# Performance work log

Hardware: AMD Instinct MI355X
Metric: run time of the kernel (lower is better)

The kernel has to match this reference:

```python
import jax, jax.numpy as jnp
import numpy as np

N = 100000
E = 1600000
F = 64
OUT = 7

def setup_inputs() -> dict:
    key = jax.random.key(0)
    k1, k2, k3, k4, k5 = jax.random.split(key, 5)
    x = jax.random.normal(k1, (N, F), dtype=jnp.float32)
    edge_index = jax.random.randint(k2, (2, E), 0, N, dtype=jnp.int64)
    W_l = jax.random.normal(k3, (F, OUT), dtype=jnp.float32) / np.sqrt(F)
    b_l = jax.random.normal(k4, (OUT,), dtype=jnp.float32) * 0.01
    W_r = jax.random.normal(k5, (F, OUT), dtype=jnp.float32) / np.sqrt(F)
    return {"x": x, "edge_index": edge_index, "W_l": W_l, "b_l": b_l, "W_r": W_r}

def reference(x, edge_index, W_l, b_l, W_r):
    # PyG SAGEConv (mean aggr): out = lin_l(mean_{j in N(i)} x_j) + lin_r(x_i), then relu
    src, dst = edge_index[0], edge_index[1]
    msgs = x[src]                                            # [E, F] gather
    agg = jax.ops.segment_sum(msgs, dst, num_segments=N)     # [N, F]
    cnt = jax.ops.segment_sum(jnp.ones((E,), dtype=x.dtype), dst, num_segments=N)
    mean = agg / jnp.maximum(cnt, 1.0)[:, None]              # isolated nodes -> 0
    out = mean @ W_l + b_l + x @ W_r                         # [N, 7]
    return jax.nn.relu(out)
```

## Files before the change

kernel.cpp:

```cpp
#include <hip/hip_runtime.h>

#define NN 100000
#define NE 1600000
#define FIN 64
#define FOUT 7

#define BSH 9
#define NBK 196
#define PBLK 2000
#define PTH  256
#define EPB  800
#define NCOPY 4
#define NCTR (NBK * NCOPY)
#define ROWS 200
#define SPLIT 4
#define NTASK (NBK * SPLIT)
#define RPS (PBLK / SPLIT)
#define ATH 512
#define WSLOT 12
#define OVCAP 256
#define SCAP 3968
#define PROJB 391
#define INVALID 0xFFFFFFFFu

__device__ __forceinline__ unsigned bf16r(float f) {
    unsigned u = __float_as_uint(f);
    return (u + 0x7fffu + ((u >> 16) & 1u)) >> 16;
}
__device__ __forceinline__ float bflo(unsigned u) { return __uint_as_float(u << 16); }
__device__ __forceinline__ float bfhi(unsigned u) { return __uint_as_float(u & 0xffff0000u); }

__global__ __launch_bounds__(256) void proj_kernel(
    const float* __restrict__ x, const float* __restrict__ Wl,
    const float* __restrict__ bl, const float* __restrict__ Wr,
    unsigned* __restrict__ z, float* __restrict__ outself, int n)
{
    int i = blockIdx.x * blockDim.x + threadIdx.x;
    if (i >= n) return;

    float al[FOUT], ar[FOUT];
#pragma unroll
    for (int j = 0; j < FOUT; ++j) { al[j] = 0.f; ar[j] = 0.f; }

    const float4* xr = (const float4*)(x + (size_t)i * FIN);
#pragma unroll
    for (int kk = 0; kk < FIN / 4; ++kk) {
        float4 xv = xr[kk];
        float v[4] = {xv.x, xv.y, xv.z, xv.w};
#pragma unroll
        for (int c = 0; c < 4; ++c) {
            int k = kk * 4 + c;
#pragma unroll
            for (int j = 0; j < FOUT; ++j) {
                al[j] = fmaf(v[c], Wl[k * FOUT + j], al[j]);
                ar[j] = fmaf(v[c], Wr[k * FOUT + j], ar[j]);
            }
        }
    }

    uint4 pk;
    pk.x = bf16r(al[0]) | (bf16r(al[1]) << 16);
    pk.y = bf16r(al[2]) | (bf16r(al[3]) << 16);
    pk.z = bf16r(al[4]) | (bf16r(al[5]) << 16);
    pk.w = bf16r(al[6]);
    ((uint4*)z)[i] = pk;

    float* o = outself + (size_t)i * FOUT;
#pragma unroll
    for (int j = 0; j < FOUT; ++j)
        o[j] = ar[j] + bl[j];
}

__global__ __launch_bounds__(PTH) void part_kernel(
    const int* __restrict__ eg, unsigned* __restrict__ part,
    unsigned short* __restrict__ offs)
{
    __shared__ unsigned st_cnt[NCTR];
    __shared__ unsigned st_start[NCTR];
    __shared__ unsigned stage[EPB];
    __shared__ unsigned wsum[NCOPY];

    const int t    = threadIdx.x;
    const int e0   = (int)blockIdx.x * EPB;
    const int lane = t & 63;
    const int wv   = t >> 6;

    for (int b = t; b < NCTR; b += PTH) st_cnt[b] = 0;
    __syncthreads();

    unsigned held[4], hcr[4];
#pragma unroll
    for (int q = 0; q < 4; ++q) hcr[q] = INVALID;
    if (t < EPB / 4) {
        uint4 S = *(const uint4*)(eg + e0 + 4 * t);
        uint4 D = *(const uint4*)(eg + NE + e0 + 4 * t);
        unsigned ss[4] = {S.x, S.y, S.z, S.w};
        unsigned dd[4] = {D.x, D.y, D.z, D.w};
#pragma unroll
        for (int q = 0; q < 4; ++q) {
            unsigned b = dd[q] >> BSH;
            unsigned cidx = (unsigned)wv * NBK + b;
            unsigned r = atomicAdd(&st_cnt[cidx], 1u);
            held[q] = ((dd[q] & 511u) << 17) | ss[q];
            hcr[q]  = (cidx << 10) | r;
        }
    }
    __syncthreads();

    unsigned c[4], p[4], tot = 0;
    if (t < NBK) {
#pragma unroll
        for (int w = 0; w < NCOPY; ++w) c[w] = st_cnt[w * NBK + t];
        p[0] = 0; p[1] = c[0]; p[2] = c[0] + c[1]; p[3] = p[2] + c[2];
        tot = p[3] + c[3];
    }
    unsigned inc = tot;
#pragma unroll
    for (int off = 1; off < 64; off <<= 1) {
        unsigned v = (unsigned)__shfl_up((int)inc, off, 64);
        if (lane >= off) inc += v;
    }
    if (lane == 63) wsum[wv] = inc;
    __syncthreads();
    if (t == 0) {
        unsigned run = 0;
#pragma unroll
        for (int w = 0; w < NCOPY; ++w) { unsigned tmp = wsum[w]; wsum[w] = run; run += tmp; }
    }
    __syncthreads();
    unsigned bstart = wsum[wv] + inc - tot;
    if (t < NBK) {
        offs[(size_t)blockIdx.x * ROWS + t] = (unsigned short)bstart;
#pragma unroll
        for (int w = 0; w < NCOPY; ++w) st_start[w * NBK + t] = bstart + p[w];
    }
    if (t == NBK) offs[(size_t)blockIdx.x * ROWS + NBK] = (unsigned short)EPB;
    __syncthreads();

#pragma unroll
    for (int q = 0; q < 4; ++q) {
        if (hcr[q] != INVALID) {
            unsigned cidx = hcr[q] >> 10, r = hcr[q] & 0x3FFu;
            stage[st_start[cidx] + r] = held[q];
        }
    }
    __syncthreads();

    const uint4* sg = (const uint4*)stage;
    uint4* pg = (uint4*)(part + (size_t)blockIdx.x * EPB);
    for (int j = t; j < EPB / 4; j += PTH) pg[j] = sg[j];
}

__global__ __launch_bounds__(ATH) void acc_kernel(
    const unsigned short* __restrict__ offs, const unsigned* __restrict__ part,
    const unsigned* __restrict__ zb, float* __restrict__ partial)
{
    __shared__ unsigned s_cnt[512];
    __shared__ unsigned s_start[512];
    __shared__ __align__(16) unsigned sstage[SCAP + 8];
    __shared__ unsigned ovf[2 * OVCAP];
    __shared__ unsigned novf;
    __shared__ unsigned wtot[8];

    const int t    = threadIdx.x;
    const int lane = t & 63;
    const int k    = blockIdx.x >> 2;
    const int sp   = blockIdx.x & 3;

    s_cnt[t] = 0;
    if (t == 0) novf = 0;
    __syncthreads();

    unsigned rbase = 0, len = 0;
    if (t < RPS) {
        unsigned r = (unsigned)(sp * RPS + t);
        unsigned o0 = offs[(size_t)r * ROWS + k];
        unsigned o1 = offs[(size_t)r * ROWS + k + 1];
        len   = o1 - o0;
        rbase = r * EPB + o0;
    }

    unsigned sh = rbase & 3u;
    const uint4* p4 = (const uint4*)part;
    unsigned wbase = rbase >> 2;
    uint4 W0 = len ? p4[wbase]     : make_uint4(0, 0, 0, 0);
    uint4 W1 = len ? p4[wbase + 1] : make_uint4(0, 0, 0, 0);
    uint4 W2 = len ? p4[wbase + 2] : make_uint4(0, 0, 0, 0);
    unsigned win[WSLOT] = {W0.x, W0.y, W0.z, W0.w,
                           W1.x, W1.y, W1.z, W1.w,
                           W2.x, W2.y, W2.z, W2.w};
    unsigned hsrc[WSLOT], hnr[WSLOT];
    unsigned F = min(len, WSLOT - sh);
#pragma unroll
    for (int q = 0; q < WSLOT; ++q) {
        unsigned uq = (unsigned)q;
        if (uq >= sh && uq < sh + F) {
            unsigned e = win[q];
            unsigned node = e >> 17;
            unsigned rk = atomicAdd(&s_cnt[node], 1u);
            hsrc[q] = e & 0x1FFFFu;
            hnr[q]  = (node << 16) | rk;
        } else hnr[q] = INVALID;
    }
    for (unsigned j = F; j < len; ++j) {
        unsigned e = part[rbase + j];
        unsigned node = e >> 17;
        unsigned rk = atomicAdd(&s_cnt[node], 1u);
        unsigned pp = atomicAdd(&novf, 1u);
        if (pp < OVCAP) {
            ovf[2 * pp]     = (node << 16) | rk;
            ovf[2 * pp + 1] = e & 0x1FFFFu;
        }
    }
    __syncthreads();

    unsigned cval = s_cnt[t];
    unsigned pcnt = (cval + 3u) & ~3u;
    unsigned inc = pcnt;
#pragma unroll
    for (int off = 1; off < 64; off <<= 1) {
        unsigned v = (unsigned)__shfl_up((int)inc, off, 64);
        if (lane >= off) inc += v;
    }
    if (lane == 63) wtot[t >> 6] = inc;
    __syncthreads();
    if (t == 0) {
        unsigned run = 0;
#pragma unroll
        for (int w = 0; w < 8; ++w) { unsigned tmp = wtot[w]; wtot[w] = run; run += tmp; }
    }
    __syncthreads();
    unsigned mybase = wtot[t >> 6] + inc - pcnt;
    s_start[t] = mybase;
    __syncthreads();

#pragma unroll
    for (int q = 0; q < WSLOT; ++q) {
        if (hnr[q] != INVALID) {
            unsigned node = hnr[q] >> 16, rk = hnr[q] & 0xffffu;
            unsigned pp = s_start[node] + rk;
            if (pp < SCAP) sstage[pp] = hsrc[q];
        }
    }
    for (unsigned q = t; q < min(novf, (unsigned)OVCAP); q += ATH) {
        unsigned nr = ovf[2 * q], src = ovf[2 * q + 1];
        unsigned pp = s_start[nr >> 16] + (nr & 0xffffu);
        if (pp < SCAP) sstage[pp] = src;
    }
    __syncthreads();

    unsigned deg = s_cnt[t];
    uint4 C0 = *(const uint4*)&sstage[mybase];
    uint4 C1 = *(const uint4*)&sstage[mybase + 4];
    unsigned sv[8] = {C0.x, C0.y, C0.z, C0.w, C1.x, C1.y, C1.z, C1.w};

    float a0 = 0.f, a1 = 0.f, a2 = 0.f, a3 = 0.f, a4 = 0.f, a5 = 0.f, a6 = 0.f;
#pragma unroll
    for (int j = 0; j < 8; ++j) {
        unsigned src = ((unsigned)j < deg) ? sv[j] : 0u;
        float m = ((unsigned)j < deg) ? 1.0f : 0.0f;
        uint4 zr = ((const uint4*)zb)[src];
        a0 = fmaf(m, bflo(zr.x), a0); a1 = fmaf(m, bfhi(zr.x), a1);
        a2 = fmaf(m, bflo(zr.y), a2); a3 = fmaf(m, bfhi(zr.y), a3);
        a4 = fmaf(m, bflo(zr.z), a4); a5 = fmaf(m, bfhi(zr.z), a5);
        a6 = fmaf(m, bflo(zr.w), a6);
    }
    for (unsigned j = 8; j < deg; ++j) {
        unsigned pp = mybase + j;
        if (pp >= SCAP) break;
        uint4 zr = ((const uint4*)zb)[sstage[pp]];
        a0 += bflo(zr.x); a1 += bfhi(zr.x);
        a2 += bflo(zr.y); a3 += bfhi(zr.y);
        a4 += bflo(zr.z); a5 += bfhi(zr.z);
        a6 += bflo(zr.w);
    }

    float* pp = partial + ((size_t)blockIdx.x * 512 + t) * 8;
    *(float4*)(pp)     = make_float4(a0, a1, a2, a3);
    *(float4*)(pp + 4) = make_float4(a4, a5, a6, (float)deg);
}

__global__ __launch_bounds__(256) void merge_kernel(
    const float* __restrict__ partial, float* __restrict__ out, int n)
{
    int i = blockIdx.x * blockDim.x + threadIdx.x;
    if (i >= n) return;
    int k = i >> BSH;
    int node = i & 511;

    float s0 = 0.f, s1 = 0.f, s2 = 0.f, s3 = 0.f, s4 = 0.f, s5 = 0.f, s6 = 0.f, cn = 0.f;
#pragma unroll
    for (int s = 0; s < SPLIT; ++s) {
        const float4* p = (const float4*)(partial + ((size_t)(k * SPLIT + s) * 512 + node) * 8);
        float4 a = p[0], b = p[1];
        s0 += a.x; s1 += a.y; s2 += a.z; s3 += a.w;
        s4 += b.x; s5 += b.y; s6 += b.z; cn += b.w;
    }
    float r = 1.0f / fmaxf(cn, 1.0f);
    float* o = out + (size_t)i * FOUT;
    o[0] = fmaxf(fmaf(s0, r, o[0]), 0.f);
    o[1] = fmaxf(fmaf(s1, r, o[1]), 0.f);
    o[2] = fmaxf(fmaf(s2, r, o[2]), 0.f);
    o[3] = fmaxf(fmaf(s3, r, o[3]), 0.f);
    o[4] = fmaxf(fmaf(s4, r, o[4]), 0.f);
    o[5] = fmaxf(fmaf(s5, r, o[5]), 0.f);
    o[6] = fmaxf(fmaf(s6, r, o[6]), 0.f);
}

extern "C" void kernel_launch(void* const* d_in, const int* in_sizes, int n_in,
                              void* d_out, int out_size, void* d_ws, size_t ws_size,
                              hipStream_t stream) {
    const float* x   = (const float*)d_in[0];
    const int*   edg = (const int*)d_in[1];
    const float* Wl  = (const float*)d_in[2];
    const float* bl  = (const float*)d_in[3];
    const float* Wr  = (const float*)d_in[4];
    float* out = (float*)d_out;

    unsigned*       z       = (unsigned*)d_ws;
    unsigned*       part    = z + (size_t)NN * 4;
    unsigned short* offs    = (unsigned short*)(part + (size_t)NE + 16);
    float*          partial = (float*)(offs + (size_t)PBLK * ROWS);

    proj_kernel<<<PROJB, 256, 0, stream>>>(x, Wl, bl, Wr, z, out, NN);
    part_kernel<<<PBLK, PTH, 0, stream>>>(edg, part, offs);
    acc_kernel<<<NTASK, ATH, 0, stream>>>(offs, part, z, partial);
    merge_kernel<<<(NN + 255) / 256, 256, 0, stream>>>(partial, out, NN);
}
```

Before: 120.7 us.

## Replace counting-sort staging in acc_kernel with shared-memory float atomic accumulation

The accumulation kernel no longer counting-sorts edges by destination node in shared memory (rank atomics, prefix scan, staging, overflow buffer) before a per-node gather loop. Each edge instead gathers its projected source row and adds the seven features plus a count into an 8x512 float shared-memory accumulator with atomicAdd. This drops several barriers, the scan and the staging capacity limits, at the cost of eight LDS float atomics per edge. Summation order becomes nondeterministic.

Result: slower. 190.5 us (+57.8%).

```diff
diff --git a/kernel.cpp b/kernel.cpp
--- a/kernel.cpp
+++ b/kernel.cpp
@@ -18,8 +18,6 @@
 #define RPS (PBLK / SPLIT)
 #define ATH 512
 #define WSLOT 12
-#define OVCAP 256
-#define SCAP 3968
 #define PROJB 391
 #define INVALID 0xFFFFFFFFu
 
@@ -151,24 +149,33 @@
     for (int j = t; j < EPB / 4; j += PTH) pg[j] = sg[j];
 }
 
+__device__ __forceinline__ void acc_edge(float (*facc)[512], const unsigned* zb,
+                                         unsigned e)
+{
+    unsigned node = e >> 17;
+    uint4 zr = ((const uint4*)zb)[e & 0x1FFFFu];
+    atomicAdd(&facc[0][node], bflo(zr.x));
+    atomicAdd(&facc[1][node], bfhi(zr.x));
+    atomicAdd(&facc[2][node], bflo(zr.y));
+    atomicAdd(&facc[3][node], bfhi(zr.y));
+    atomicAdd(&facc[4][node], bflo(zr.z));
+    atomicAdd(&facc[5][node], bfhi(zr.z));
+    atomicAdd(&facc[6][node], bflo(zr.w));
+    atomicAdd(&facc[7][node], 1.0f);
+}
+
 __global__ __launch_bounds__(ATH) void acc_kernel(
     const unsigned short* __restrict__ offs, const unsigned* __restrict__ part,
     const unsigned* __restrict__ zb, float* __restrict__ partial)
 {
-    __shared__ unsigned s_cnt[512];
-    __shared__ unsigned s_start[512];
-    __shared__ __align__(16) unsigned sstage[SCAP + 8];
-    __shared__ unsigned ovf[2 * OVCAP];
-    __shared__ unsigned novf;
-    __shared__ unsigned wtot[8];
-
-    const int t    = threadIdx.x;
-    const int lane = t & 63;
-    const int k    = blockIdx.x >> 2;
-    const int sp   = blockIdx.x & 3;
-
-    s_cnt[t] = 0;
-    if (t == 0) novf = 0;
+    __shared__ float facc[8][512];
+
+    const int t  = threadIdx.x;
+    const int k  = blockIdx.x >> 2;
+    const int sp = blockIdx.x & 3;
+
+#pragma unroll
+    for (int j = 0; j < 8; ++j) facc[j][t] = 0.f;
     __syncthreads();
 
     unsigned rbase = 0, len = 0;
@@ -189,95 +196,20 @@
     unsigned win[WSLOT] = {W0.x, W0.y, W0.z, W0.w,
                            W1.x, W1.y, W1.z, W1.w,
                            W2.x, W2.y, W2.z, W2.w};
-    unsigned hsrc[WSLOT], hnr[WSLOT];
     unsigned F = min(len, WSLOT - sh);
 #pragma unroll
     for (int q = 0; q < WSLOT; ++q) {
         unsigned uq = (unsigned)q;
-        if (uq >= sh && uq < sh + F) {
-            unsigned e = win[q];
-            unsigned node = e >> 17;
-            unsigned rk = atomicAdd(&s_cnt[node], 1u);
-            hsrc[q] = e & 0x1FFFFu;
-            hnr[q]  = (node << 16) | rk;
-        } else hnr[q] = INVALID;
-    }
-    for (unsigned j = F; j < len; ++j) {
-        unsigned e = part[rbase + j];
-        unsigned node = e >> 17;
-        unsigned rk = atomicAdd(&s_cnt[node], 1u);
-        unsigned pp = atomicAdd(&novf, 1u);
-        if (pp < OVCAP) {
-            ovf[2 * pp]     = (node << 16) | rk;
-            ovf[2 * pp + 1] = e & 0x1FFFFu;
-        }
-    }
-    __syncthreads();
-
-    unsigned cval = s_cnt[t];
-    unsigned pcnt = (cval + 3u) & ~3u;
-    unsigned inc = pcnt;
-#pragma unroll
-    for (int off = 1; off < 64; off <<= 1) {
-        unsigned v = (unsigned)__shfl_up((int)inc, off, 64);
-        if (lane >= off) inc += v;
-    }
-    if (lane == 63) wtot[t >> 6] = inc;
-    __syncthreads();
-    if (t == 0) {
-        unsigned run = 0;
-#pragma unroll
-        for (int w = 0; w < 8; ++w) { unsigned tmp = wtot[w]; wtot[w] = run; run += tmp; }
-    }
-    __syncthreads();
-    unsigned mybase = wtot[t >> 6] + inc - pcnt;
-    s_start[t] = mybase;
-    __syncthreads();
-
-#pragma unroll
-    for (int q = 0; q < WSLOT; ++q) {
-        if (hnr[q] != INVALID) {
-            unsigned node = hnr[q] >> 16, rk = hnr[q] & 0xffffu;
-            unsigned pp = s_start[node] + rk;
-            if (pp < SCAP) sstage[pp] = hsrc[q];
-        }
-    }
-    for (unsigned q = t; q < min(novf, (unsigned)OVCAP); q += ATH) {
-        unsigned nr = ovf[2 * q], src = ovf[2 * q + 1];
-        unsigned pp = s_start[nr >> 16] + (nr & 0xffffu);
-        if (pp < SCAP) sstage[pp] = src;
-    }
-    __syncthreads();
-
-    unsigned deg = s_cnt[t];
-    uint4 C0 = *(const uint4*)&sstage[mybase];
-    uint4 C1 = *(const uint4*)&sstage[mybase + 4];
-    unsigned sv[8] = {C0.x, C0.y, C0.z, C0.w, C1.x, C1.y, C1.z, C1.w};
-
-    float a0 = 0.f, a1 = 0.f, a2 = 0.f, a3 = 0.f, a4 = 0.f, a5 = 0.f, a6 = 0.f;
-#pragma unroll
-    for (int j = 0; j < 8; ++j) {
-        unsigned src = ((unsigned)j < deg) ? sv[j] : 0u;
-        float m = ((unsigned)j < deg) ? 1.0f : 0.0f;
-        uint4 zr = ((const uint4*)zb)[src];
-        a0 = fmaf(m, bflo(zr.x), a0); a1 = fmaf(m, bfhi(zr.x), a1);
-        a2 = fmaf(m, bflo(zr.y), a2); a3 = fmaf(m, bfhi(zr.y), a3);
-        a4 = fmaf(m, bflo(zr.z), a4); a5 = fmaf(m, bfhi(zr.z), a5);
-        a6 = fmaf(m, bflo(zr.w), a6);
-    }
-    for (unsigned j = 8; j < deg; ++j) {
-        unsigned pp = mybase + j;
-        if (pp >= SCAP) break;
-        uint4 zr = ((const uint4*)zb)[sstage[pp]];
-        a0 += bflo(zr.x); a1 += bfhi(zr.x);
-        a2 += bflo(zr.y); a3 += bfhi(zr.y);
-        a4 += bflo(zr.z); a5 += bfhi(zr.z);
-        a6 += bflo(zr.w);
-    }
+        if (uq >= sh && uq < sh + F)
+            acc_edge(facc, zb, win[q]);
+    }
+    for (unsigned j = F; j < len; ++j)
+        acc_edge(facc, zb, part[rbase + j]);
+    __syncthreads();
 
     float* pp = partial + ((size_t)blockIdx.x * 512 + t) * 8;
-    *(float4*)(pp)     = make_float4(a0, a1, a2, a3);
-    *(float4*)(pp + 4) = make_float4(a4, a5, a6, (float)deg);
+    *(float4*)(pp)     = make_float4(facc[0][t], facc[1][t], facc[2][t], facc[3][t]);
+    *(float4*)(pp + 4) = make_float4(facc[4][t], facc[5][t], facc[6][t], facc[7][t]);
 }
 
 __global__ __launch_bounds__(256) void merge_kernel(
```

## Replace shared-memory atomic counting sort with per-wave ballot match histograms

Applied to the files above, without the earlier changes.

The in-block bucketing of edges by destination node no longer uses a shared atomicAdd per edge. Each wavefront instead computes a match mask with 9 ballots, takes intra-wave ranks with popcount, and keeps a private histogram per wave; the per-wave counts are summed and scanned afterwards. The aim is to remove contention and serialization from LDS atomics. In exchange it adds about ten ballots per slot, eight histograms of LDS, and a tail loop that runs to the wave's maximum length.

Result: slower. 130.0 us (+7.7%).

```diff
diff --git a/kernel.cpp b/kernel.cpp
--- a/kernel.cpp
+++ b/kernel.cpp
@@ -30,6 +30,17 @@
 __device__ __forceinline__ float bflo(unsigned u) { return __uint_as_float(u << 16); }
 __device__ __forceinline__ float bfhi(unsigned u) { return __uint_as_float(u & 0xffff0000u); }
 
+template <int BITS>
+__device__ __forceinline__ unsigned long long matchmask(unsigned n, bool v) {
+    unsigned long long m = __ballot(v ? 1 : 0);
+#pragma unroll
+    for (int b = 0; b < BITS; ++b) {
+        unsigned long long bb = __ballot((int)((n >> b) & 1u));
+        m &= ((n >> b) & 1u) ? bb : ~bb;
+    }
+    return m;
+}
+
 __global__ __launch_bounds__(256) void proj_kernel(
     const float* __restrict__ x, const float* __restrict__ Wl,
     const float* __restrict__ bl, const float* __restrict__ Wr,
@@ -155,8 +166,7 @@
     const unsigned short* __restrict__ offs, const unsigned* __restrict__ part,
     const unsigned* __restrict__ zb, float* __restrict__ partial)
 {
-    __shared__ unsigned s_cnt[512];
-    __shared__ unsigned s_start[512];
+    __shared__ unsigned hist[8][512];
     __shared__ __align__(16) unsigned sstage[SCAP + 8];
     __shared__ unsigned ovf[2 * OVCAP];
     __shared__ unsigned novf;
@@ -164,10 +174,13 @@
 
     const int t    = threadIdx.x;
     const int lane = t & 63;
+    const int wv   = t >> 6;
     const int k    = blockIdx.x >> 2;
     const int sp   = blockIdx.x & 3;
-
-    s_cnt[t] = 0;
+    const unsigned long long lmlt = (1ull << lane) - 1ull;
+
+#pragma unroll
+    for (int w = 0; w < 8; ++w) hist[w][t] = 0;
     if (t == 0) novf = 0;
     __syncthreads();
 
@@ -189,33 +202,52 @@
     unsigned win[WSLOT] = {W0.x, W0.y, W0.z, W0.w,
                            W1.x, W1.y, W1.z, W1.w,
                            W2.x, W2.y, W2.z, W2.w};
-    unsigned hsrc[WSLOT], hnr[WSLOT];
     unsigned F = min(len, WSLOT - sh);
+    unsigned rkw[WSLOT];
+    bool     vl[WSLOT];
 #pragma unroll
     for (int q = 0; q < WSLOT; ++q) {
         unsigned uq = (unsigned)q;
-        if (uq >= sh && uq < sh + F) {
-            unsigned e = win[q];
-            unsigned node = e >> 17;
-            unsigned rk = atomicAdd(&s_cnt[node], 1u);
-            hsrc[q] = e & 0x1FFFFu;
-            hnr[q]  = (node << 16) | rk;
-        } else hnr[q] = INVALID;
-    }
-    for (unsigned j = F; j < len; ++j) {
-        unsigned e = part[rbase + j];
-        unsigned node = e >> 17;
-        unsigned rk = atomicAdd(&s_cnt[node], 1u);
-        unsigned pp = atomicAdd(&novf, 1u);
-        if (pp < OVCAP) {
-            ovf[2 * pp]     = (node << 16) | rk;
-            ovf[2 * pp + 1] = e & 0x1FFFFu;
-        }
-    }
-    __syncthreads();
-
-    unsigned cval = s_cnt[t];
-    unsigned pcnt = (cval + 3u) & ~3u;
+        bool v = (uq >= sh) && (uq < sh + F);
+        vl[q] = v;
+        unsigned n = win[q] >> 17;
+        unsigned long long m = matchmask<9>(n, v);
+        unsigned rkr = __popcll(m & lmlt);
+        unsigned cnr = __popcll(m);
+        unsigned cur = v ? hist[wv][n] : 0u;
+        if (v && rkr == 0) hist[wv][n] = cur + cnr;
+        rkw[q] = cur + rkr;
+    }
+    {
+        unsigned tail = len - F;
+        unsigned tmax = tail;
+#pragma unroll
+        for (int off = 32; off >= 1; off >>= 1)
+            tmax = max(tmax, (unsigned)__shfl_xor((int)tmax, off, 64));
+        for (unsigned jj = 0; jj < tmax; ++jj) {
+            bool v = (jj < tail);
+            unsigned e = v ? part[rbase + F + jj] : 0u;
+            unsigned n = e >> 17;
+            unsigned long long m = matchmask<9>(n, v);
+            unsigned rkr = __popcll(m & lmlt);
+            unsigned cnr = __popcll(m);
+            unsigned cur = v ? hist[wv][n] : 0u;
+            if (v && rkr == 0) hist[wv][n] = cur + cnr;
+            if (v) {
+                unsigned p = atomicAdd(&novf, 1u);
+                if (p < OVCAP) {
+                    ovf[2 * p]     = ((unsigned)wv << 28) | (n << 16) | (cur + rkr);
+                    ovf[2 * p + 1] = e & 0x1FFFFu;
+                }
+            }
+        }
+    }
+    __syncthreads();
+
+    unsigned wbs[8], tot = 0;
+#pragma unroll
+    for (int w = 0; w < 8; ++w) { wbs[w] = tot; tot += hist[w][t]; }
+    unsigned pcnt = (tot + 3u) & ~3u;
     unsigned inc = pcnt;
 #pragma unroll
     for (int off = 1; off < 64; off <<= 1) {
@@ -231,25 +263,26 @@
     }
     __syncthreads();
     unsigned mybase = wtot[t >> 6] + inc - pcnt;
-    s_start[t] = mybase;
+#pragma unroll
+    for (int w = 0; w < 8; ++w) hist[w][t] = mybase + wbs[w];
     __syncthreads();
 
 #pragma unroll
     for (int q = 0; q < WSLOT; ++q) {
-        if (hnr[q] != INVALID) {
-            unsigned node = hnr[q] >> 16, rk = hnr[q] & 0xffffu;
-            unsigned pp = s_start[node] + rk;
-            if (pp < SCAP) sstage[pp] = hsrc[q];
+        if (vl[q]) {
+            unsigned n = win[q] >> 17;
+            unsigned pp = hist[wv][n] + rkw[q];
+            if (pp < SCAP) sstage[pp] = win[q] & 0x1FFFFu;
         }
     }
     for (unsigned q = t; q < min(novf, (unsigned)OVCAP); q += ATH) {
-        unsigned nr = ovf[2 * q], src = ovf[2 * q + 1];
-        unsigned pp = s_start[nr >> 16] + (nr & 0xffffu);
+        unsigned a = ovf[2 * q], src = ovf[2 * q + 1];
+        unsigned pp = hist[a >> 28][(a >> 16) & 0x1FFu] + (a & 0xFFFFu);
         if (pp < SCAP) sstage[pp] = src;
     }
     __syncthreads();
 
-    unsigned deg = s_cnt[t];
+    unsigned deg = tot;
     uint4 C0 = *(const uint4*)&sstage[mybase];
     uint4 C1 = *(const uint4*)&sstage[mybase + 4];
     unsigned sv[8] = {C0.x, C0.y, C0.z, C0.w, C1.x, C1.y, C1.z, C1.w};
```
